# Optimization experiments

Hardware: AMD Instinct MI355X
Metric: run time of the kernel (lower is better)

Reference implementation:

```python
import jax, jax.numpy as jnp
import numpy as np

MERSENNE_P = (1 << 31) - 1  # prime used by universal hashing


def _uhash_cols(random_numbers, n_full_cols, n_comp_cols):
    """Universal-hash map from full-weight column index -> compressed column index.
    h(j) = ((r0*j + r1) mod P) mod n_comp_cols  (ints stay well within int64).
    """
    j = jnp.arange(n_full_cols, dtype=jnp.int64)
    r0 = random_numbers[0]
    r1 = random_numbers[1]
    return ((r0 * j + r1) % MERSENNE_P) % n_comp_cols


def setup_inputs() -> dict:
    key = jax.random.key(0)
    k1, k2, k3 = jax.random.split(key, 3)
    in_features, out_features, redn_factor = 8192, 8192, 4
    init_scale = 1.0 / np.sqrt(in_features)
    x = jax.random.normal(k1, (64, in_features), dtype=jnp.float32)
    weight = jax.random.uniform(
        k2, (out_features, in_features // redn_factor), dtype=jnp.float32,
        minval=-init_scale, maxval=init_scale)
    random_numbers = jax.random.randint(k3, (4,), 1, 1048576, dtype=jnp.int64)
    return {"x": x, "weight": weight, "random_numbers": random_numbers,
            "redn_factor": 4}


def reference(x, weight, random_numbers, redn_factor):
    # x: [..., K]; weight (compressed): [N, K // redn_factor]
    orig_shape = x.shape
    K = orig_shape[-1]
    x2d = x.reshape(-1, K)                      # preprocess: flatten leading dims
    n_comp = weight.shape[1]
    col_idx = _uhash_cols(random_numbers, K, n_comp)   # [K] hashed gather indices
    w_full = weight[:, col_idx]                 # [N, K] expanded via hashed gather
    y = x2d @ w_full.T                          # [rows, N]
    return y.reshape(*orig_shape[:-1], y.shape[-1])  # postprocess
```

## Files before the change

### kernel.cpp

```cpp
#include <hip/hip_runtime.h>
#include <hip/hip_bf16.h>

#define K_FULL   8192
#define M_ROWS   64
#define N_OUT    8192
#define N_COMP   2048
#define P_MERS   2147483647


typedef __attribute__((ext_vector_type(8))) short bf16x8;
typedef __attribute__((ext_vector_type(4))) float f32x4;

__device__ __forceinline__ short f2bfs(float f) {
    __hip_bfloat16 h = __float2bfloat16(f);
    return *reinterpret_cast<short*>(&h);
}
__device__ __forceinline__ unsigned int pk2bf(float a, float b) {
    return (unsigned int)(unsigned short)f2bfs(a)
         | ((unsigned int)(unsigned short)f2bfs(b) << 16);
}

__device__ __forceinline__ int hash_col(int j, int rn0, int rn1, int rn2, int rn3) {
    if (rn1 == 0 && rn3 == 0) {
        unsigned long long xx = (unsigned long long)(unsigned int)rn0 * (unsigned int)j
                              + (unsigned long long)(unsigned int)rn2;
        unsigned long long t = (xx & (unsigned long long)P_MERS) + (xx >> 31);
        if (t >= (unsigned long long)P_MERS) t -= (unsigned long long)P_MERS;
        return (int)(t & (N_COMP - 1));
    } else {
        unsigned int t = (unsigned int)rn0 * (unsigned int)j + (unsigned int)rn1;
        int ti = (int)t;
        int m1 = ti % P_MERS;
        if (m1 < 0) m1 += P_MERS;
        return m1 & (N_COMP - 1);
    }
}

__global__ __launch_bounds__(1024) void k_xc(const float* __restrict__ x,
                                             const int* __restrict__ rn,
                                             unsigned int* __restrict__ xcF) {
    __shared__ float row[N_COMP];
    const int m = blockIdx.x;
    const int tid = threadIdx.x;
    row[tid] = 0.0f;
    row[tid + 1024] = 0.0f;
    const int rn0 = rn[0], rn1 = rn[1], rn2 = rn[2], rn3 = rn[3];
    __syncthreads();

    const float* xm = x + (size_t)m * K_FULL;
#pragma unroll
    for (int it = 0; it < 2; ++it) {
        int j0 = tid * 4 + it * 4096;
        float4 v = *(const float4*)(xm + j0);
        atomicAdd(&row[hash_col(j0 + 0, rn0, rn1, rn2, rn3)], v.x);
        atomicAdd(&row[hash_col(j0 + 1, rn0, rn1, rn2, rn3)], v.y);
        atomicAdd(&row[hash_col(j0 + 2, rn0, rn1, rn2, rn3)], v.z);
        atomicAdd(&row[hash_col(j0 + 3, rn0, rn1, rn2, rn3)], v.w);
    }
    __syncthreads();

    const int c0 = 2 * tid;
    const int s  = c0 >> 5;
    const int kg = (c0 >> 3) & 3;
    const int e0 = c0 & 7;
    const int g  = m >> 4;
    const int nr = m & 15;
    xcF[(((s * 4 + g) * 64 + kg * 16 + nr) << 2) + (e0 >> 1)] =
        pk2bf(row[c0], row[c0 + 1]);
}

#define WROWD 132

__global__ __launch_bounds__(512) void k_gemm(const float* __restrict__ W,
                                              const unsigned short* __restrict__ xcF,
                                              float* __restrict__ y) {
    __shared__ unsigned int wt[2][16 * WROWD];
    __shared__ float ys[8][M_ROWS][16];
    const int tid  = threadIdx.x;
    const int lane = tid & 63;
    const int w    = __builtin_amdgcn_readfirstlane(tid >> 6);
    const int nr   = lane & 15;
    const int kg   = lane >> 4;
    const int n0   = blockIdx.x * 16;
    const int rot  = (blockIdx.x >> 3) & 7;
    const int r0   = 2 * w;

    const float* wrow = W + (size_t)(n0 + r0) * N_COMP;
    const unsigned short* ab = xcF + (size_t)w * 2048 + lane * 8;

    f32x4 acc0 = {0.f, 0.f, 0.f, 0.f};
    f32x4 acc1 = {0.f, 0.f, 0.f, 0.f};
    f32x4 acc2 = {0.f, 0.f, 0.f, 0.f};
    f32x4 acc3 = {0.f, 0.f, 0.f, 0.f};

    {
        float4 va = *(const float4*)(wrow + rot * 256 + lane * 4);
        float4 vb = *(const float4*)(wrow + rot * 256 + N_COMP + lane * 4);
        uint2 pa = { pk2bf(va.x, va.y), pk2bf(va.z, va.w) };
        uint2 pb = { pk2bf(vb.x, vb.y), pk2bf(vb.z, vb.w) };
        *(uint2*)&wt[0][r0 * WROWD + lane * 2]       = pa;
        *(uint2*)&wt[0][(r0 + 1) * WROWD + lane * 2] = pb;
    }
    const unsigned short* ap0 = ab + (size_t)rot * 16384;
    bf16x8 a0 = *(const bf16x8*)(ap0);
    bf16x8 a1 = *(const bf16x8*)(ap0 + 512);
    bf16x8 a2 = *(const bf16x8*)(ap0 + 1024);
    bf16x8 a3 = *(const bf16x8*)(ap0 + 1536);
    __syncthreads();

#pragma unroll 1
    for (int p = 0; p < 8; ++p) {
        const int b  = p & 1;
        const int pn = (p + 1 + rot) & 7;
        float4 nva, nvb;
        bf16x8 na0, na1, na2, na3;
        if (p < 7) {
            nva = *(const float4*)(wrow + pn * 256 + lane * 4);
            nvb = *(const float4*)(wrow + pn * 256 + N_COMP + lane * 4);
            const unsigned short* nab = ab + (size_t)pn * 16384;
            na0 = *(const bf16x8*)(nab);
            na1 = *(const bf16x8*)(nab + 512);
            na2 = *(const bf16x8*)(nab + 1024);
            na3 = *(const bf16x8*)(nab + 1536);
        }
        bf16x8 bf = *(const bf16x8*)((const unsigned short*)&wt[b][0]
                                     + nr * (WROWD * 2) + w * 32 + kg * 8);
        acc0 = __builtin_amdgcn_mfma_f32_16x16x32_bf16(a0, bf, acc0, 0, 0, 0);
        acc1 = __builtin_amdgcn_mfma_f32_16x16x32_bf16(a1, bf, acc1, 0, 0, 0);
        acc2 = __builtin_amdgcn_mfma_f32_16x16x32_bf16(a2, bf, acc2, 0, 0, 0);
        acc3 = __builtin_amdgcn_mfma_f32_16x16x32_bf16(a3, bf, acc3, 0, 0, 0);
        if (p < 7) {
            uint2 pa = { pk2bf(nva.x, nva.y), pk2bf(nva.z, nva.w) };
            uint2 pb = { pk2bf(nvb.x, nvb.y), pk2bf(nvb.z, nvb.w) };
            *(uint2*)&wt[b ^ 1][r0 * WROWD + lane * 2]       = pa;
            *(uint2*)&wt[b ^ 1][(r0 + 1) * WROWD + lane * 2] = pb;
            a0 = na0; a1 = na1; a2 = na2; a3 = na3;
        }
        __syncthreads();
    }

#pragma unroll
    for (int j = 0; j < 4; ++j) {
        ys[w][ 0 + kg * 4 + j][nr] = acc0[j];
        ys[w][16 + kg * 4 + j][nr] = acc1[j];
        ys[w][32 + kg * 4 + j][nr] = acc2[j];
        ys[w][48 + kg * 4 + j][nr] = acc3[j];
    }
    __syncthreads();

#pragma unroll
    for (int i = 0; i < 2; ++i) {
        int o = tid + 512 * i;
        int m = o >> 4;
        int n = o & 15;
        float s = 0.f;
#pragma unroll
        for (int q = 0; q < 8; ++q) s += ys[q][m][n];
        y[(size_t)m * N_OUT + n0 + n] = s;
    }
}

extern "C" void kernel_launch(void* const* d_in, const int* in_sizes, int n_in,
                              void* d_out, int out_size, void* d_ws, size_t ws_size,
                              hipStream_t stream) {
    const float* x = (const float*)d_in[0];
    const float* W = (const float*)d_in[1];
    const int* rn  = (const int*)d_in[2];
    float* y       = (float*)d_out;

    unsigned int* xcF = (unsigned int*)d_ws;

    k_xc<<<M_ROWS, 1024, 0, stream>>>(x, rn, xcF);
    k_gemm<<<N_OUT / 16, 512, 0, stream>>>(W, (const unsigned short*)xcF, y);
}
```

Measured before the change: 30.68 us.

## Stream weight tiles directly into LDS via global_load_lds, convert to bf16 on read

Weight tiles now go from global memory straight into shared memory through the direct global-to-LDS load, stored as fp32, and are converted to bf16 when read for the MFMA. Activation fragments are no longer prefetched into registers one step ahead; they are loaded inside each iteration. The goal is to cut the register round trip and the VGPR pressure of the staging path. In exchange the kernel needs twice the LDS for the weight tile, does redundant conversions on read, and loses the activation prefetch. Correctness also relies on the barrier covering completion of the async LDS loads (vmcnt).

```diff
diff --git a/kernel.cpp b/kernel.cpp
--- a/kernel.cpp
+++ b/kernel.cpp
@@ -19,6 +19,10 @@
     return (unsigned int)(unsigned short)f2bfs(a)
          | ((unsigned int)(unsigned short)f2bfs(b) << 16);
 }
+
+#define GLL(g, l) __builtin_amdgcn_global_load_lds(                          \
+    (const __attribute__((address_space(1))) unsigned int*)(g),             \
+    (__attribute__((address_space(3))) unsigned int*)(l), 16, 0, 0)
 
 __device__ __forceinline__ int hash_col(int j, int rn0, int rn1, int rn2, int rn3) {
     if (rn1 == 0 && rn3 == 0) {
@@ -69,12 +73,13 @@
         pk2bf(row[c0], row[c0 + 1]);
 }
 
-#define WROWD 132
+#define WT_ROWD 260
+#define WT_TILE (16 * WT_ROWD)
 
 __global__ __launch_bounds__(512) void k_gemm(const float* __restrict__ W,
                                               const unsigned short* __restrict__ xcF,
                                               float* __restrict__ y) {
-    __shared__ unsigned int wt[2][16 * WROWD];
+    __shared__ float wt[2][WT_TILE];
     __shared__ float ys[8][M_ROWS][16];
     const int tid  = threadIdx.x;
     const int lane = tid & 63;
@@ -85,7 +90,8 @@
     const int rot  = (blockIdx.x >> 3) & 7;
     const int r0   = 2 * w;
 
-    const float* wrow = W + (size_t)(n0 + r0) * N_COMP;
+    const float* g0 = W + (size_t)(n0 + r0) * N_COMP + lane * 4;
+    const float* g1 = g0 + N_COMP;
     const unsigned short* ab = xcF + (size_t)w * 2048 + lane * 8;
 
     f32x4 acc0 = {0.f, 0.f, 0.f, 0.f};
@@ -93,49 +99,36 @@
     f32x4 acc2 = {0.f, 0.f, 0.f, 0.f};
     f32x4 acc3 = {0.f, 0.f, 0.f, 0.f};
 
-    {
-        float4 va = *(const float4*)(wrow + rot * 256 + lane * 4);
-        float4 vb = *(const float4*)(wrow + rot * 256 + N_COMP + lane * 4);
-        uint2 pa = { pk2bf(va.x, va.y), pk2bf(va.z, va.w) };
-        uint2 pb = { pk2bf(vb.x, vb.y), pk2bf(vb.z, vb.w) };
-        *(uint2*)&wt[0][r0 * WROWD + lane * 2]       = pa;
-        *(uint2*)&wt[0][(r0 + 1) * WROWD + lane * 2] = pb;
-    }
-    const unsigned short* ap0 = ab + (size_t)rot * 16384;
-    bf16x8 a0 = *(const bf16x8*)(ap0);
-    bf16x8 a1 = *(const bf16x8*)(ap0 + 512);
-    bf16x8 a2 = *(const bf16x8*)(ap0 + 1024);
-    bf16x8 a3 = *(const bf16x8*)(ap0 + 1536);
+    GLL(g0 + rot * 256, &wt[0][r0 * WT_ROWD]);
+    GLL(g1 + rot * 256, &wt[0][(r0 + 1) * WT_ROWD]);
     __syncthreads();
 
 #pragma unroll 1
     for (int p = 0; p < 8; ++p) {
         const int b  = p & 1;
+        const int pm = (p + rot) & 7;
         const int pn = (p + 1 + rot) & 7;
-        float4 nva, nvb;
-        bf16x8 na0, na1, na2, na3;
         if (p < 7) {
-            nva = *(const float4*)(wrow + pn * 256 + lane * 4);
-            nvb = *(const float4*)(wrow + pn * 256 + N_COMP + lane * 4);
-            const unsigned short* nab = ab + (size_t)pn * 16384;
-            na0 = *(const bf16x8*)(nab);
-            na1 = *(const bf16x8*)(nab + 512);
-            na2 = *(const bf16x8*)(nab + 1024);
-            na3 = *(const bf16x8*)(nab + 1536);
+            GLL(g0 + pn * 256, &wt[b ^ 1][r0 * WT_ROWD]);
+            GLL(g1 + pn * 256, &wt[b ^ 1][(r0 + 1) * WT_ROWD]);
         }
-        bf16x8 bf = *(const bf16x8*)((const unsigned short*)&wt[b][0]
-                                     + nr * (WROWD * 2) + w * 32 + kg * 8);
+        const unsigned short* ap = ab + (size_t)pm * 16384;
+        bf16x8 a0 = *(const bf16x8*)(ap);
+        bf16x8 a1 = *(const bf16x8*)(ap + 512);
+        bf16x8 a2 = *(const bf16x8*)(ap + 1024);
+        bf16x8 a3 = *(const bf16x8*)(ap + 1536);
+        const float* bp = &wt[b][nr * WT_ROWD + w * 32 + kg * 8];
+        float4 f0 = *(const float4*)(bp);
+        float4 f1 = *(const float4*)(bp + 4);
+        bf16x8 bf;
+        bf[0] = f2bfs(f0.x); bf[1] = f2bfs(f0.y);
+        bf[2] = f2bfs(f0.z); bf[3] = f2bfs(f0.w);
+        bf[4] = f2bfs(f1.x); bf[5] = f2bfs(f1.y);
+        bf[6] = f2bfs(f1.z); bf[7] = f2bfs(f1.w);
         acc0 = __builtin_amdgcn_mfma_f32_16x16x32_bf16(a0, bf, acc0, 0, 0, 0);
         acc1 = __builtin_amdgcn_mfma_f32_16x16x32_bf16(a1, bf, acc1, 0, 0, 0);
         acc2 = __builtin_amdgcn_mfma_f32_16x16x32_bf16(a2, bf, acc2, 0, 0, 0);
         acc3 = __builtin_amdgcn_mfma_f32_16x16x32_bf16(a3, bf, acc3, 0, 0, 0);
-        if (p < 7) {
-            uint2 pa = { pk2bf(nva.x, nva.y), pk2bf(nva.z, nva.w) };
-            uint2 pb = { pk2bf(nvb.x, nvb.y), pk2bf(nvb.z, nvb.w) };
-            *(uint2*)&wt[b ^ 1][r0 * WROWD + lane * 2]       = pa;
-            *(uint2*)&wt[b ^ 1][(r0 + 1) * WROWD + lane * 2] = pb;
-            a0 = na0; a1 = na1; a2 = na2; a3 = na3;
-        }
         __syncthreads();
     }
 
```

Measured after the change: 30.76 us. No clear change (+0.3%).
